# Performance work log

Hardware: AMD Instinct MI355X
Metric: run time of the kernel (lower is better)

The kernel has to match this reference:

```python
import jax, jax.numpy as jnp
import numpy as np

# --- Mamba2Simple hyperparams (derived from init_kwargs) ---
D_MODEL = 2048
D_STATE = 128
HEADDIM = 64
EXPAND = 2
D_CONV = 4
NGROUPS = 1
CHUNK = 256
EPS = 1e-5
D_INNER = EXPAND * D_MODEL            # 4096
NHEADS = D_INNER // HEADDIM           # 64
CONV_DIM = D_INNER + 2 * NGROUPS * D_STATE          # 4352
D_IN_PROJ = 2 * D_INNER + 2 * NGROUPS * D_STATE + NHEADS  # 8512


def setup_inputs() -> dict:
    key = jax.random.key(0)
    ks = jax.random.split(key, 9)
    B, L = 2, 2048
    x = jax.random.normal(ks[0], (B, L, D_MODEL), jnp.float32)
    w_in = jax.random.normal(ks[1], (D_MODEL, D_IN_PROJ), jnp.float32) * (D_MODEL ** -0.5)
    conv_w = jax.random.normal(ks[2], (CONV_DIM, D_CONV), jnp.float32) * 0.2
    conv_b = jnp.zeros((CONV_DIM,), jnp.float32)
    dt_bias = jax.random.uniform(ks[3], (NHEADS,), jnp.float32, -4.0, -1.0)
    # A in [1, 16] per official init -> A_log = log(A)
    A_log = jnp.log(jax.random.uniform(ks[4], (NHEADS,), jnp.float32, 1.0, 16.0))
    D = jnp.ones((NHEADS,), jnp.float32)
    norm_w = jnp.ones((D_INNER,), jnp.float32)
    w_out = jax.random.normal(ks[5], (D_INNER, D_MODEL), jnp.float32) * (D_INNER ** -0.5)
    return {"x": x, "w_in": w_in, "conv_w": conv_w, "conv_b": conv_b,
            "dt_bias": dt_bias, "A_log": A_log, "D": D, "norm_w": norm_w, "w_out": w_out}


def _segsum(a):
    # a: (..., T) -> (..., T, T) with out[i, j] = sum_{k=j+1..i} a[k] for j<=i else -inf
    T = a.shape[-1]
    cs = jnp.cumsum(a, axis=-1)
    d = cs[..., :, None] - cs[..., None, :]
    mask = jnp.tril(jnp.ones((T, T), dtype=bool))
    return jnp.where(mask, d, -jnp.inf)


def _ssd(X, A, Bm, Cm):
    # X: (b, l, h, p) already multiplied by dt; A: (b, l, h) = dt*A_cont
    # Bm, Cm: (b, l, n)  (ngroups=1, broadcast over heads)
    b, l, h, p = X.shape
    n = Bm.shape[-1]
    c = l // CHUNK
    X = X.reshape(b, c, CHUNK, h, p)
    A = A.reshape(b, c, CHUNK, h).transpose(0, 3, 1, 2)      # (b, h, c, q)
    Bm = Bm.reshape(b, c, CHUNK, n)
    Cm = Cm.reshape(b, c, CHUNK, n)
    A_cs = jnp.cumsum(A, axis=-1)                             # (b, h, c, q)
    Lmat = jnp.exp(_segsum(A))                                # (b, h, c, q, q)
    # intra-chunk (diagonal block) output
    Y_diag = jnp.einsum("bcln,bcsn,bhcls,bcshp->bclhp", Cm, Bm, Lmat, X)
    # per-chunk final states
    decay_states = jnp.exp(A_cs[..., -1:] - A_cs)             # (b, h, c, q)
    states = jnp.einsum("bcln,bhcl,bclhp->bchpn", Bm, decay_states, X)
    # inter-chunk recurrence
    A_last = jnp.pad(A_cs[..., -1], ((0, 0), (0, 0), (1, 0)))  # (b, h, c+1)
    decay_chunk = jnp.exp(_segsum(A_last))                     # (b, h, c+1, c+1)
    states = jnp.concatenate([jnp.zeros_like(states[:, :1]), states], axis=1)
    states = jnp.einsum("bhzc,bchpn->bzhpn", decay_chunk, states)[:, :-1]
    # state -> output contribution
    Y_off = jnp.einsum("bchpn,bcln,bhcl->bclhp", states, Cm, jnp.exp(A_cs))
    return (Y_diag + Y_off).reshape(b, l, h, p)


def _mamba2(x, w_in, conv_w, conv_b, dt_bias, A_log, D, norm_w, w_out):
    B, L, _ = x.shape
    zxbcdt = jnp.einsum("bld,de->ble", x, w_in)               # (B, L, 8512)
    z = zxbcdt[..., :D_INNER]
    xBC = zxbcdt[..., D_INNER:D_INNER + CONV_DIM]
    dt = zxbcdt[..., D_INNER + CONV_DIM:]                      # (B, L, H)
    dt = jax.nn.softplus(dt + dt_bias)
    # causal depthwise conv1d + silu
    xp = jnp.pad(xBC, ((0, 0), (D_CONV - 1, 0), (0, 0)))
    acc = conv_b
    xBC = sum(conv_w[:, k] * xp[:, k:k + L, :] for k in range(D_CONV)) + conv_b
    xBC = jax.nn.silu(xBC)
    xh = xBC[..., :D_INNER].reshape(B, L, NHEADS, HEADDIM)
    Bm = xBC[..., D_INNER:D_INNER + NGROUPS * D_STATE]         # (B, L, N) since ngroups=1
    Cm = xBC[..., D_INNER + NGROUPS * D_STATE:]                # (B, L, N)
    A = -jnp.exp(A_log)                                        # (H,)
    y = _ssd(xh * dt[..., None], dt * A, Bm, Cm)               # (B, L, H, P)
    y = y + xh * D[None, None, :, None]                        # skip term
    y = y.reshape(B, L, D_INNER)
    # gated RMSNorm (norm_before_gate=False): normalize(y * silu(z)) * weight
    y = y * jax.nn.silu(z)
    y = y * jax.lax.rsqrt(jnp.mean(y * y, axis=-1, keepdims=True) + EPS) * norm_w
    return jnp.einsum("ble,ed->bld", y, w_out)


def reference(x, w_in, conv_w, conv_b, dt_bias, A_log, D, norm_w, w_out):
    return x + _mamba2(x, w_in, conv_w, conv_b, dt_bias, A_log, D, norm_w, w_out)
```

## Files before the change

kernel.cpp:

```cpp
#include <hip/hip_runtime.h>
#include <math.h>

#define DEV __device__ __forceinline__

typedef __attribute__((ext_vector_type(4))) float f32x4;
typedef __attribute__((ext_vector_type(4))) unsigned short u16x4;
typedef __attribute__((ext_vector_type(8))) unsigned short u16x8;
typedef __attribute__((ext_vector_type(8))) __bf16 bfv8;

DEV unsigned short f2bf(float f) {
  unsigned u = __builtin_bit_cast(unsigned, f);
  u = (u + 0x7FFFu + ((u >> 16) & 1u)) >> 16;
  return (unsigned short)u;
}
DEV float bf2f(unsigned short h) {
  unsigned u = ((unsigned)h) << 16;
  return __builtin_bit_cast(float, u);
}

DEV f32x4 mfma16(u16x8 a, u16x8 b, f32x4 c) {
  return __builtin_amdgcn_mfma_f32_16x16x32_bf16(
      __builtin_bit_cast(bfv8, a), __builtin_bit_cast(bfv8, b), c, 0, 0, 0);
}

DEV void gload_lds16(const unsigned short* g, unsigned short* s) {
  __builtin_amdgcn_global_load_lds(
      (const __attribute__((address_space(1))) void*)g,
      (__attribute__((address_space(3))) void*)s, 16, 0, 0);
}

template <int N>
DEV void vmcnt_wait() {
  if constexpr (N == 0) asm volatile("s_waitcnt vmcnt(0)" ::: "memory");
  else if constexpr (N == 2) asm volatile("s_waitcnt vmcnt(2)" ::: "memory");
  else if constexpr (N == 4) asm volatile("s_waitcnt vmcnt(4)" ::: "memory");
}

__global__ __launch_bounds__(512, 2) void gemm8_in(
    const unsigned short* __restrict__ A, const unsigned short* __restrict__ Bt,
    unsigned short* __restrict__ o_z, unsigned short* __restrict__ o_xbc,
    float* __restrict__ o_dt) {
  constexpr int K = 2048, NT = K / 64;
  __shared__ __align__(16) unsigned short As[2][256 * 64];
  __shared__ __align__(16) unsigned short Bs[2][256 * 64];
  const int tid = threadIdx.x;
  const int lane = tid & 63, w = tid >> 6;
  const int l16 = lane & 15, lq = lane >> 4;
  const int wr = w >> 1, wc = w & 1;
  const int nwg = gridDim.x * gridDim.y;
  int lin = blockIdx.y * gridDim.x + blockIdx.x;
  lin = (lin & 7) * (nwg >> 3) + (lin >> 3);
  const int m0 = (lin / gridDim.x) * 256, n0 = (lin % gridDim.x) * 256;
  const int srow = lane >> 3;
  const int schk = (lane & 7) ^ srow;
  const unsigned short* Ag = A + (size_t)(m0 + srow) * K + schk * 8;
  const unsigned short* Bg = Bt + (size_t)(n0 + srow) * K + schk * 8;
  const int px0 = lq ^ (l16 & 7);
  const int px1 = (4 + lq) ^ (l16 & 7);

  f32x4 acc[4][8] = {};

  auto stageA = [&](int p, int slot, int kt) {
    gload_lds16(Ag + (size_t)(slot * 64 + w * 8) * K + kt * 64,
                &As[p][(slot * 64 + w * 8) * 64]);
  };
  auto stageB = [&](int p, int slot, int kt) {
    gload_lds16(Bg + (size_t)(slot * 64 + w * 8) * K + kt * 64,
                &Bs[p][(slot * 64 + w * 8) * 64]);
  };
  auto rdA = [&](int p, int mf, int k2) -> u16x8 {
    const int row = wr * 64 + mf * 16 + l16;
    return *(const u16x8*)(&As[p][row * 64 + (k2 ? px1 : px0) * 8]);
  };
  auto rdB = [&](int p, int nf, int k2) -> u16x8 {
    const int row = wc * 128 + nf * 16 + l16;
    return *(const u16x8*)(&Bs[p][row * 64 + (k2 ? px1 : px0) * 8]);
  };

  stageA(0, 0, 0); stageA(0, 1, 0); stageA(0, 2, 0); stageA(0, 3, 0);
  stageB(0, 0, 0); stageB(0, 2, 0); stageB(0, 1, 0); stageB(0, 3, 0);
  vmcnt_wait<2>();
  __builtin_amdgcn_s_barrier();

  u16x8 a0[4], a1[4], b0[2], b1[2];
  for (int k = 0; k < NT; ++k) {
    const int p = k & 1, pn = p ^ 1;
    const bool st = (k + 1 < NT);
#pragma unroll
    for (int mf = 0; mf < 4; ++mf) { a0[mf] = rdA(p, mf, 0); a1[mf] = rdA(p, mf, 1); }
    b0[0] = rdB(p, 0, 0); b1[0] = rdB(p, 0, 1);
    b0[1] = rdB(p, 1, 0); b1[1] = rdB(p, 1, 1);
    if (st) { stageA(pn, 0, k + 1); stageA(pn, 1, k + 1); }
    __builtin_amdgcn_s_barrier();
    __builtin_amdgcn_s_setprio(1);
#pragma unroll
    for (int nf = 0; nf < 2; ++nf)
#pragma unroll
      for (int mf = 0; mf < 4; ++mf) {
        acc[mf][nf] = mfma16(a0[mf], b0[nf], acc[mf][nf]);
        acc[mf][nf] = mfma16(a1[mf], b1[nf], acc[mf][nf]);
      }
    __builtin_amdgcn_s_setprio(0);
    __builtin_amdgcn_s_barrier();
    b0[0] = rdB(p, 2, 0); b1[0] = rdB(p, 2, 1);
    b0[1] = rdB(p, 3, 0); b1[1] = rdB(p, 3, 1);
    if (st) { stageA(pn, 2, k + 1); stageA(pn, 3, k + 1); vmcnt_wait<4>(); }
    else vmcnt_wait<0>();
    __builtin_amdgcn_s_barrier();
    __builtin_amdgcn_s_setprio(1);
#pragma unroll
    for (int nf = 0; nf < 2; ++nf)
#pragma unroll
      for (int mf = 0; mf < 4; ++mf) {
        acc[mf][2 + nf] = mfma16(a0[mf], b0[nf], acc[mf][2 + nf]);
        acc[mf][2 + nf] = mfma16(a1[mf], b1[nf], acc[mf][2 + nf]);
      }
    __builtin_amdgcn_s_setprio(0);
    __builtin_amdgcn_s_barrier();
    b0[0] = rdB(p, 4, 0); b1[0] = rdB(p, 4, 1);
    b0[1] = rdB(p, 5, 0); b1[1] = rdB(p, 5, 1);
    if (st) { stageB(pn, 0, k + 1); stageB(pn, 2, k + 1); }
    __builtin_amdgcn_s_barrier();
    __builtin_amdgcn_s_setprio(1);
#pragma unroll
    for (int nf = 0; nf < 2; ++nf)
#pragma unroll
      for (int mf = 0; mf < 4; ++mf) {
        acc[mf][4 + nf] = mfma16(a0[mf], b0[nf], acc[mf][4 + nf]);
        acc[mf][4 + nf] = mfma16(a1[mf], b1[nf], acc[mf][4 + nf]);
      }
    __builtin_amdgcn_s_setprio(0);
    __builtin_amdgcn_s_barrier();
    b0[0] = rdB(p, 6, 0); b1[0] = rdB(p, 6, 1);
    b0[1] = rdB(p, 7, 0); b1[1] = rdB(p, 7, 1);
    if (st) { stageB(pn, 1, k + 1); stageB(pn, 3, k + 1); vmcnt_wait<2>(); }
    else vmcnt_wait<0>();
    __builtin_amdgcn_s_barrier();
    __builtin_amdgcn_s_setprio(1);
#pragma unroll
    for (int nf = 0; nf < 2; ++nf)
#pragma unroll
      for (int mf = 0; mf < 4; ++mf) {
        acc[mf][6 + nf] = mfma16(a0[mf], b0[nf], acc[mf][6 + nf]);
        acc[mf][6 + nf] = mfma16(a1[mf], b1[nf], acc[mf][6 + nf]);
      }
    __builtin_amdgcn_s_setprio(0);
    __builtin_amdgcn_s_barrier();
  }

#pragma unroll
  for (int mf = 0; mf < 4; ++mf) {
#pragma unroll
    for (int nf = 0; nf < 8; ++nf) {
      const int col = n0 + wc * 128 + nf * 16 + l16;
#pragma unroll
      for (int r = 0; r < 4; ++r) {
        const int row = m0 + wr * 64 + mf * 16 + lq * 4 + r;
        float v = acc[mf][nf][r];
        if (col < 4096) o_z[(size_t)row * 4096 + col] = f2bf(v);
        else if (col < 8448) o_xbc[(size_t)row * 4352 + (col - 4096)] = f2bf(v);
        else if (col < 8512) o_dt[(size_t)row * 64 + (col - 8448)] = v;
      }
    }
  }
}

__global__ __launch_bounds__(256, 3) void gemm_p(
    const unsigned short* __restrict__ A, const unsigned short* __restrict__ Bt,
    int K, float* __restrict__ o_c, const float* __restrict__ resid) {
  __shared__ __align__(16) unsigned short As[3][128 * 32];
  __shared__ __align__(16) unsigned short Bs[3][128 * 32];
  const int tid = threadIdx.x;
  const int lane = tid & 63, w = tid >> 6;
  const int l16 = lane & 15, lq = lane >> 4;
  const int wr = w >> 1, wc = w & 1;
  const int nwg = gridDim.x * gridDim.y;
  int lin = blockIdx.y * gridDim.x + blockIdx.x;
  lin = (lin & 7) * (nwg >> 3) + (lin >> 3);
  const int m0 = (lin / gridDim.x) * 128, n0 = (lin % gridDim.x) * 128;
  const int lrow = lane >> 2;
  const int gq = (lane & 3) ^ ((lrow >> 1) & 3);
  const int cq = lq ^ ((l16 >> 1) & 3);

  const unsigned short* Ag = A + (size_t)(m0 + lrow) * K + gq * 8;
  const unsigned short* Bg = Bt + (size_t)(n0 + lrow) * K + gq * 8;

  f32x4 acc[4][4] = {};

  auto stage = [&](int bi, int kt) {
#pragma unroll
    for (int i = 0; i < 2; ++i) {
      const int rb = (w + i * 4) * 16;
      gload_lds16(Ag + (size_t)rb * K + kt * 32, &As[bi][rb * 32]);
    }
#pragma unroll
    for (int i = 0; i < 2; ++i) {
      const int rb = (w + i * 4) * 16;
      gload_lds16(Bg + (size_t)rb * K + kt * 32, &Bs[bi][rb * 32]);
    }
  };

  const int nt = K / 32;
  stage(0, 0);
  stage(1, 1);

  for (int k = 0; k < nt; ++k) {
    const int cb = k % 3;
    if (k < nt - 1) vmcnt_wait<4>();
    else vmcnt_wait<0>();
    __builtin_amdgcn_s_barrier();
    if (k + 2 < nt) stage((k + 2) % 3, k + 2);

    u16x8 af[4], bf[4];
#pragma unroll
    for (int mf = 0; mf < 4; ++mf)
      af[mf] = *(const u16x8*)(&As[cb][(wr * 64 + mf * 16 + l16) * 32 + cq * 8]);
#pragma unroll
    for (int nf = 0; nf < 4; ++nf)
      bf[nf] = *(const u16x8*)(&Bs[cb][(wc * 64 + nf * 16 + l16) * 32 + cq * 8]);

    __builtin_amdgcn_s_setprio(1);
#pragma unroll
    for (int mf = 0; mf < 4; ++mf)
#pragma unroll
      for (int nf = 0; nf < 4; ++nf)
        acc[mf][nf] = mfma16(af[mf], bf[nf], acc[mf][nf]);
    __builtin_amdgcn_s_setprio(0);
  }

#pragma unroll
  for (int mf = 0; mf < 4; ++mf) {
#pragma unroll
    for (int nf = 0; nf < 4; ++nf) {
      const int col = n0 + wc * 64 + nf * 16 + l16;
#pragma unroll
      for (int r = 0; r < 4; ++r) {
        const int row = m0 + wr * 64 + mf * 16 + lq * 4 + r;
        size_t idx = (size_t)row * 2048 + col;
        o_c[idx] = acc[mf][nf][r] + resid[idx];
      }
    }
  }
}

__global__ __launch_bounds__(256) void prep_kernel(
    const float* __restrict__ x, unsigned short* __restrict__ xbf,
    const float* __restrict__ w_in, unsigned short* __restrict__ w_inT) {
  __shared__ __align__(16) unsigned short T[64][72];
  const int b = blockIdx.x;
  const int tid = threadIdx.x;
  if (b < 4096) {
    const size_t i = ((size_t)b * 256 + tid) * 8;
    f32x4 a = *(const f32x4*)(x + i);
    f32x4 c = *(const f32x4*)(x + i + 4);
    u16x8 o;
#pragma unroll
    for (int j = 0; j < 4; ++j) { o[j] = f2bf(a[j]); o[j + 4] = f2bf(c[j]); }
    *(u16x8*)(xbf + i) = o;
  } else {
    const int idx = b - 4096;
    const int c0 = (idx % 136) * 64, r0 = (idx / 136) * 64;
#pragma unroll
    for (int it = 0; it < 4; ++it) {
      int r = it * 16 + (tid >> 4);
      int c = (tid & 15) * 4;
      f32x4 v = {0.f, 0.f, 0.f, 0.f};
      if (c0 + c < 8512) v = *(const f32x4*)(w_in + (size_t)(r0 + r) * 8512 + c0 + c);
#pragma unroll
      for (int j = 0; j < 4; ++j) T[c + j][r] = f2bf(v[j]);
    }
    __syncthreads();
    const int nr = tid >> 2, kc = (tid & 3) * 16;
    u16x8 a = *(const u16x8*)(&T[nr][kc]);
    u16x8 c = *(const u16x8*)(&T[nr][kc + 8]);
    unsigned short* o = w_inT + (size_t)(c0 + nr) * 2048 + r0 + kc;
    *(u16x8*)o = a;
    *(u16x8*)(o + 8) = c;
  }
}

__global__ __launch_bounds__(256) void transpose_conv(
    const float* __restrict__ in, unsigned short* __restrict__ out, int R,
    int C) {
  __shared__ __align__(16) unsigned short T[64][72];
  const int c0 = blockIdx.x * 64, r0 = blockIdx.y * 64;
  const int tid = threadIdx.x;
#pragma unroll
  for (int it = 0; it < 4; ++it) {
    int r = it * 16 + (tid >> 4);
    int c = (tid & 15) * 4;
    f32x4 v = {0.f, 0.f, 0.f, 0.f};
    if (c0 + c < C) v = *(const f32x4*)(in + (size_t)(r0 + r) * C + c0 + c);
#pragma unroll
    for (int j = 0; j < 4; ++j) T[c + j][r] = f2bf(v[j]);
  }
  __syncthreads();
  const int nr = tid >> 2, kc = (tid & 3) * 16;
  u16x8 a = *(const u16x8*)(&T[nr][kc]);
  u16x8 b = *(const u16x8*)(&T[nr][kc + 8]);
  unsigned short* o = out + (size_t)(c0 + nr) * R + r0 + kc;
  *(u16x8*)o = a;
  *(u16x8*)(o + 8) = b;
}

__global__ __launch_bounds__(256) void convdt_kernel(
    const unsigned short* __restrict__ raw, const float* __restrict__ cw,
    const float* __restrict__ cb, unsigned short* __restrict__ xbc,
    float* __restrict__ dtb, const float* __restrict__ dt_bias,
    const float* __restrict__ A_log, float* __restrict__ Acs) {
  __shared__ float wsum[4];
  const int b = blockIdx.x;
  const int tid = threadIdx.x;
  if (b < 5120) {
    const int ch4 = (b % 5) * 256 + tid;
    if (ch4 >= 1088) return;
    const int ch = ch4 * 4;
    const int r0 = (b / 5) * 4;
    const int l0 = r0 & 2047;
    f32x4 w0 = *(const f32x4*)(cw + ch * 4);
    f32x4 w1 = *(const f32x4*)(cw + ch * 4 + 4);
    f32x4 w2 = *(const f32x4*)(cw + ch * 4 + 8);
    f32x4 w3 = *(const f32x4*)(cw + ch * 4 + 12);
    f32x4 bias = *(const f32x4*)(cb + ch);
    f32x4 v[7];
#pragma unroll
    for (int i = 0; i < 7; ++i) {
      if (l0 - 3 + i >= 0) {
        u16x4 h = *(const u16x4*)(raw + (size_t)(r0 - 3 + i) * 4352 + ch);
        v[i] = (f32x4){bf2f(h[0]), bf2f(h[1]), bf2f(h[2]), bf2f(h[3])};
      } else {
        v[i] = (f32x4){0.f, 0.f, 0.f, 0.f};
      }
    }
#pragma unroll
    for (int j = 0; j < 4; ++j) {
      f32x4 acc = bias;
#pragma unroll
      for (int k = 0; k < 4; ++k) {
        acc[0] += w0[k] * v[j + k][0];
        acc[1] += w1[k] * v[j + k][1];
        acc[2] += w2[k] * v[j + k][2];
        acc[3] += w3[k] * v[j + k][3];
      }
      u16x4 o;
#pragma unroll
      for (int q = 0; q < 4; ++q) {
        float s = acc[q] / (1.0f + __expf(-acc[q]));
        o[q] = f2bf(s);
      }
      *(u16x4*)(xbc + (size_t)(r0 + j) * 4352 + ch) = o;
    }
  } else {
    const int blk = b - 5120;
    const int c = blk & 7, h = (blk >> 3) & 63, bb = blk >> 9;
    const int lane = tid & 63, w = tid >> 6;
    const int row = bb * 2048 + c * 256 + tid;
    float xv = dtb[(size_t)row * 64 + h] + dt_bias[h];
    float dt = (xv > 20.0f) ? xv : log1pf(__expf(xv));
    dtb[(size_t)row * 64 + h] = dt;
    float s = dt * (-__expf(A_log[h]));
#pragma unroll
    for (int off = 1; off < 64; off <<= 1) {
      float v = __shfl_up(s, off, 64);
      if (lane >= off) s += v;
    }
    if (lane == 63) wsum[w] = s;
    __syncthreads();
    float base = 0.0f;
#pragma unroll
    for (int i = 0; i < 4; ++i)
      if (i < w) base += wsum[i];
    Acs[((size_t)((bb * 64 + h) * 8 + c)) * 256 + tid] = s + base;
  }
}

__global__ __launch_bounds__(256) void g_kernel(
    const unsigned short* __restrict__ xbc, float* __restrict__ G) {
  const int bc = blockIdx.y;
  const int i0 = (blockIdx.x >> 2) * 64, j0 = (blockIdx.x & 3) * 64;
  const int tid = threadIdx.x;
  const int lane = tid & 63, w = tid >> 6;
  const int l16 = lane & 15, lq = lane >> 4;
  const unsigned short* base = xbc + (size_t)bc * 256 * 4352;
  f32x4 acc[4] = {};
#pragma unroll
  for (int ks = 0; ks < 4; ++ks) {
    int nb = ks * 32 + lq * 8;
    u16x8 af = *(const u16x8*)(base + (size_t)(i0 + w * 16 + l16) * 4352 + 4224 + nb);
#pragma unroll
    for (int jf = 0; jf < 4; ++jf) {
      u16x8 bb = *(const u16x8*)(base + (size_t)(j0 + jf * 16 + l16) * 4352 + 4096 + nb);
      acc[jf] = mfma16(af, bb, acc[jf]);
    }
  }
  float* Gt = G + (size_t)bc * 65536;
#pragma unroll
  for (int jf = 0; jf < 4; ++jf)
#pragma unroll
    for (int r = 0; r < 4; ++r)
      Gt[(i0 + w * 16 + lq * 4 + r) * 256 + j0 + jf * 16 + l16] = acc[jf][r];
}

__global__ __launch_bounds__(512) void ssd_states(
    const unsigned short* __restrict__ xbc, const float* __restrict__ dtb,
    const float* __restrict__ Acs, unsigned short* __restrict__ statesb) {
  __shared__ __align__(16) unsigned short Xt[64 * 264];
  __shared__ __align__(16) unsigned short BmT[128 * 72];
  __shared__ float As_s[256];
  const int h = blockIdx.x, c = blockIdx.y, b = blockIdx.z;
  const int tid = threadIdx.x;
  const int lane = tid & 63, w = tid >> 6;
  const int l16 = lane & 15, lq = lane >> 4;
  const int row0 = b * 2048 + c * 256;

  if (tid < 256) As_s[tid] = Acs[((size_t)((b * 64 + h) * 8 + c)) * 256 + tid];
#pragma unroll
  for (int it = 0; it < 2; ++it) {
    int pb = tid & 15;
    int tb = it * 32 + (tid >> 4);
    float rr[4][4];
#pragma unroll
    for (int i = 0; i < 4; ++i) {
      int row = row0 + tb * 4 + i;
      u16x4 v = *(const u16x4*)(xbc + (size_t)row * 4352 + h * 64 + pb * 4);
      float dtv = dtb[(size_t)row * 64 + h];
#pragma unroll
      for (int j = 0; j < 4; ++j) rr[i][j] = bf2f(v[j]) * dtv;
    }
#pragma unroll
    for (int j = 0; j < 4; ++j) {
      u16x4 hh = {f2bf(rr[0][j]), f2bf(rr[1][j]), f2bf(rr[2][j]), f2bf(rr[3][j])};
      *(u16x4*)(&Xt[(pb * 4 + j) * 264 + tb * 4]) = hh;
    }
  }
  __syncthreads();

  f32x4 accS[4] = {};
  const float Alast = As_s[255];
  for (int part = 0; part < 4; ++part) {
    if (part) __syncthreads();
    {
      int nb = tid & 31;
      int tb = tid >> 5;
      float rr[4][4];
#pragma unroll
      for (int i = 0; i < 4; ++i) {
        int t = part * 64 + tb * 4 + i;
        int row = row0 + t;
        float dec = __expf(Alast - As_s[t]);
        u16x4 v = *(const u16x4*)(xbc + (size_t)row * 4352 + 4096 + nb * 4);
#pragma unroll
        for (int j = 0; j < 4; ++j) rr[i][j] = bf2f(v[j]) * dec;
      }
#pragma unroll
      for (int j = 0; j < 4; ++j) {
        u16x4 hh = {f2bf(rr[0][j]), f2bf(rr[1][j]), f2bf(rr[2][j]), f2bf(rr[3][j])};
        *(u16x4*)(&BmT[(nb * 4 + j) * 72 + tb * 4]) = hh;
      }
    }
    __syncthreads();
#pragma unroll
    for (int ks = 0; ks < 2; ++ks) {
      int toff = ks * 32 + lq * 8;
      u16x8 af = *(const u16x8*)(&BmT[(w * 16 + l16) * 72 + toff]);
#pragma unroll
      for (int pf = 0; pf < 4; ++pf) {
        u16x8 bfr = *(const u16x8*)(&Xt[(pf * 16 + l16) * 264 + part * 64 + toff]);
        accS[pf] = mfma16(af, bfr, accS[pf]);
      }
    }
  }
  unsigned short* Sp = statesb + (size_t)((b * 8 + c) * 64 + h) * 8192;
#pragma unroll
  for (int pf = 0; pf < 4; ++pf) {
    u16x4 hh = {f2bf(accS[pf][0]), f2bf(accS[pf][1]), f2bf(accS[pf][2]),
                f2bf(accS[pf][3])};
    *(u16x4*)(&Sp[(pf * 16 + l16) * 128 + w * 16 + lq * 4]) = hh;
  }
}

__global__ __launch_bounds__(256) void scan_states(
    const unsigned short* __restrict__ statesb, const float* __restrict__ Acs,
    unsigned short* __restrict__ prefix) {
  const int h = blockIdx.x, b = blockIdx.y;
  const int tid = threadIdx.x;
  const int p = tid >> 2, nq = (tid & 3) * 32;
  float S[32];
#pragma unroll
  for (int i = 0; i < 32; ++i) S[i] = 0.0f;
  for (int cc = 0; cc < 8; ++cc) {
    size_t base = (size_t)((b * 8 + cc) * 64 + h) * 8192 + p * 128 + nq;
#pragma unroll
    for (int j = 0; j < 4; ++j) {
      u16x8 hh;
#pragma unroll
      for (int k = 0; k < 8; ++k) hh[k] = f2bf(S[j * 8 + k]);
      *(u16x8*)(prefix + base + j * 8) = hh;
    }
    float eAl = __expf(Acs[((size_t)((b * 64 + h) * 8 + cc)) * 256 + 255]);
#pragma unroll
    for (int j = 0; j < 4; ++j) {
      u16x8 v = *(const u16x8*)(statesb + base + j * 8);
#pragma unroll
      for (int k = 0; k < 8; ++k) S[j * 8 + k] = eAl * S[j * 8 + k] + bf2f(v[k]);
    }
  }
}

__global__ __launch_bounds__(512) void ssd_main(
    const unsigned short* __restrict__ xbc, const float* __restrict__ dtb,
    const float* __restrict__ Acs, const float* __restrict__ G,
    const unsigned short* __restrict__ prefix, const float* __restrict__ Dv,
    unsigned short* __restrict__ y) {
  __shared__ __align__(16) unsigned short Xt[64 * 264];
  __shared__ float As_s[256];
  const int h = blockIdx.x, c = blockIdx.y, b = blockIdx.z;
  const int tid = threadIdx.x;
  const int lane = tid & 63, w = tid >> 6;
  const int l16 = lane & 15, lq = lane >> 4;
  const int row0 = b * 2048 + c * 256;

  if (tid < 256) As_s[tid] = Acs[((size_t)((b * 64 + h) * 8 + c)) * 256 + tid];
#pragma unroll
  for (int it = 0; it < 2; ++it) {
    int pb = tid & 15;
    int tb = it * 32 + (tid >> 4);
    float rr[4][4];
#pragma unroll
    for (int i = 0; i < 4; ++i) {
      int row = row0 + tb * 4 + i;
      u16x4 v = *(const u16x4*)(xbc + (size_t)row * 4352 + h * 64 + pb * 4);
      float dtv = dtb[(size_t)row * 64 + h];
#pragma unroll
      for (int j = 0; j < 4; ++j) rr[i][j] = bf2f(v[j]) * dtv;
    }
#pragma unroll
    for (int j = 0; j < 4; ++j) {
      u16x4 hh = {f2bf(rr[0][j]), f2bf(rr[1][j]), f2bf(rr[2][j]), f2bf(rr[3][j])};
      *(u16x4*)(&Xt[(pb * 4 + j) * 264 + tb * 4]) = hh;
    }
  }
  __syncthreads();

  f32x4 acc[2][4] = {};
  const float* Gt = G + (size_t)(b * 8 + c) * 65536;
  for (int ks = 0; ks < 8; ++ks) {
    const int tb = ks * 32 + lq * 8;
    u16x8 bfr[4];
#pragma unroll
    for (int pf = 0; pf < 4; ++pf)
      bfr[pf] = *(const u16x8*)(&Xt[(pf * 16 + l16) * 264 + tb]);
#pragma unroll
    for (int mf = 0; mf < 2; ++mf) {
      const int i = w * 32 + mf * 16 + l16;
      const float ai = As_s[i];
      const float* gp = Gt + i * 256 + tb;
      f32x4 g0 = *(const f32x4*)gp;
      f32x4 g1 = *(const f32x4*)(gp + 4);
      u16x8 af;
#pragma unroll
      for (int jj = 0; jj < 8; ++jj) {
        int j = tb + jj;
        float g = (jj < 4) ? g0[jj] : g1[jj - 4];
        float v = (i >= j) ? g * __expf(ai - As_s[j]) : 0.0f;
        af[jj] = f2bf(v);
      }
#pragma unroll
      for (int pf = 0; pf < 4; ++pf)
        acc[mf][pf] = mfma16(af, bfr[pf], acc[mf][pf]);
    }
  }
  const unsigned short* Pf = prefix + (size_t)((b * 8 + c) * 64 + h) * 8192;
  for (int ks = 0; ks < 4; ++ks) {
    const int nb = ks * 32 + lq * 8;
    u16x8 bfr[4];
#pragma unroll
    for (int pf = 0; pf < 4; ++pf)
      bfr[pf] = *(const u16x8*)(Pf + (size_t)(pf * 16 + l16) * 128 + nb);
#pragma unroll
    for (int mf = 0; mf < 2; ++mf) {
      const int i = w * 32 + mf * 16 + l16;
      const float eAi = __expf(As_s[i]);
      u16x8 cv = *(const u16x8*)(xbc + (size_t)(row0 + i) * 4352 + 4224 + nb);
      u16x8 af;
#pragma unroll
      for (int jj = 0; jj < 8; ++jj) af[jj] = f2bf(bf2f(cv[jj]) * eAi);
#pragma unroll
      for (int pf = 0; pf < 4; ++pf)
        acc[mf][pf] = mfma16(af, bfr[pf], acc[mf][pf]);
    }
  }
  const float Dh = Dv[h];
#pragma unroll
  for (int mf = 0; mf < 2; ++mf) {
#pragma unroll
    for (int r = 0; r < 4; ++r) {
      int t = w * 32 + mf * 16 + lq * 4 + r;
      size_t row = (size_t)(row0 + t);
#pragma unroll
      for (int pf = 0; pf < 4; ++pf) {
        int p = pf * 16 + l16;
        float xh = bf2f(xbc[row * 4352 + h * 64 + p]);
        y[row * 4096 + h * 64 + p] = f2bf(acc[mf][pf][r] + Dh * xh);
      }
    }
  }
}

__global__ __launch_bounds__(256) void norm_kernel(
    unsigned short* __restrict__ y, const unsigned short* __restrict__ zbf,
    const float* __restrict__ nw) {
  const int row = blockIdx.x, tid = threadIdx.x;
  unsigned short* yr = y + (size_t)row * 4096;
  const unsigned short* zr = zbf + (size_t)row * 4096;
  float vals[16];
  float ss = 0.0f;
#pragma unroll
  for (int i = 0; i < 2; ++i) {
    int cb = i * 2048 + tid * 8;
    u16x8 yv = *(const u16x8*)(yr + cb);
    u16x8 zv = *(const u16x8*)(zr + cb);
#pragma unroll
    for (int j = 0; j < 8; ++j) {
      float z = bf2f(zv[j]);
      float g = bf2f(yv[j]) * (z / (1.0f + __expf(-z)));
      vals[i * 8 + j] = g;
      ss += g * g;
    }
  }
#pragma unroll
  for (int off = 32; off > 0; off >>= 1) ss += __shfl_xor(ss, off, 64);
  __shared__ float red[4];
  if ((tid & 63) == 0) red[tid >> 6] = ss;
  __syncthreads();
  float tot = red[0] + red[1] + red[2] + red[3];
  float rr = rsqrtf(tot * (1.0f / 4096.0f) + 1e-5f);
#pragma unroll
  for (int i = 0; i < 2; ++i) {
    int cb = i * 2048 + tid * 8;
    f32x4 w0 = *(const f32x4*)(nw + cb);
    f32x4 w1 = *(const f32x4*)(nw + cb + 4);
    u16x8 o;
#pragma unroll
    for (int j = 0; j < 8; ++j) {
      float wv = (j < 4) ? w0[j] : w1[j - 4];
      o[j] = f2bf(vals[i * 8 + j] * rr * wv);
    }
    *(u16x8*)(yr + cb) = o;
  }
}

extern "C" void kernel_launch(void* const* d_in, const int* in_sizes, int n_in,
                              void* d_out, int out_size, void* d_ws,
                              size_t ws_size, hipStream_t stream) {
  const float* x = (const float*)d_in[0];
  const float* w_in = (const float*)d_in[1];
  const float* conv_w = (const float*)d_in[2];
  const float* conv_b = (const float*)d_in[3];
  const float* dt_bias = (const float*)d_in[4];
  const float* A_log = (const float*)d_in[5];
  const float* Dvec = (const float*)d_in[6];
  const float* norm_w = (const float*)d_in[7];
  const float* w_out = (const float*)d_in[8];
  float* out = (float*)d_out;

  char* w = (char*)d_ws;
  unsigned short* zbf = (unsigned short*)(w + 0);
  unsigned short* xbc = (unsigned short*)(w + 33554432);
  unsigned short* xbcraw = (unsigned short*)(w + 69206016);
  float* dtb = (float*)(w + 104857600);
  float* Acs = (float*)(w + 105906176);
  float* G = (float*)(w + 106954752);
  unsigned short* statesb = (unsigned short*)(w + 111149056);
  unsigned short* y = (unsigned short*)(w + 127926272);
  unsigned short* xbf = (unsigned short*)(w + 111149056);
  unsigned short* w_inT = (unsigned short*)(w + 33554432);
  unsigned short* w_outT = (unsigned short*)(w + 33554432);
  unsigned short* prefix = xbcraw;

  prep_kernel<<<dim3(8448), 256, 0, stream>>>(x, xbf, w_in, w_inT);
  gemm8_in<<<dim3(34, 16), 512, 0, stream>>>(xbf, w_inT, zbf, xbcraw, dtb);
  convdt_kernel<<<dim3(6144), 256, 0, stream>>>(xbcraw, conv_w, conv_b, xbc,
                                                dtb, dt_bias, A_log, Acs);
  g_kernel<<<dim3(16, 16), 256, 0, stream>>>(xbc, G);
  ssd_states<<<dim3(64, 8, 2), 512, 0, stream>>>(xbc, dtb, Acs, statesb);
  scan_states<<<dim3(64, 2), 256, 0, stream>>>(statesb, Acs, prefix);
  ssd_main<<<dim3(64, 8, 2), 512, 0, stream>>>(xbc, dtb, Acs, G, prefix, Dvec, y);
  transpose_conv<<<dim3(32, 64), 256, 0, stream>>>(w_out, w_outT, 4096, 2048);
  norm_kernel<<<dim3(4096), 256, 0, stream>>>(y, zbf, norm_w);
  gemm_p<<<dim3(16, 32), 256, 0, stream>>>(y, w_outT, 4096, out, x);
}
```

Measured before the change: 460.7 us.

## Store G in bf16, split state scan across N halves, fuse norm with w_out transpose

The intra-chunk C·B^T matrix G is now written and read as bf16 instead of fp32, halving its memory traffic in g_kernel and ssd_main. The state scan is split into two blocks per head along the state dimension, doubling parallelism with fewer registers per thread. The w_out transpose is merged into the RMSNorm launch as extra blocks, removing one kernel launch and letting both run concurrently. Rounding G to bf16 adds a small precision loss before the decay multiply.

Result: faster. 436.4 us (-5.3%).

```diff
diff --git a/kernel.cpp b/kernel.cpp
--- a/kernel.cpp
+++ b/kernel.cpp
@@ -279,30 +279,6 @@
   }
 }
 
-__global__ __launch_bounds__(256) void transpose_conv(
-    const float* __restrict__ in, unsigned short* __restrict__ out, int R,
-    int C) {
-  __shared__ __align__(16) unsigned short T[64][72];
-  const int c0 = blockIdx.x * 64, r0 = blockIdx.y * 64;
-  const int tid = threadIdx.x;
-#pragma unroll
-  for (int it = 0; it < 4; ++it) {
-    int r = it * 16 + (tid >> 4);
-    int c = (tid & 15) * 4;
-    f32x4 v = {0.f, 0.f, 0.f, 0.f};
-    if (c0 + c < C) v = *(const f32x4*)(in + (size_t)(r0 + r) * C + c0 + c);
-#pragma unroll
-    for (int j = 0; j < 4; ++j) T[c + j][r] = f2bf(v[j]);
-  }
-  __syncthreads();
-  const int nr = tid >> 2, kc = (tid & 3) * 16;
-  u16x8 a = *(const u16x8*)(&T[nr][kc]);
-  u16x8 b = *(const u16x8*)(&T[nr][kc + 8]);
-  unsigned short* o = out + (size_t)(c0 + nr) * R + r0 + kc;
-  *(u16x8*)o = a;
-  *(u16x8*)(o + 8) = b;
-}
-
 __global__ __launch_bounds__(256) void convdt_kernel(
     const unsigned short* __restrict__ raw, const float* __restrict__ cw,
     const float* __restrict__ cb, unsigned short* __restrict__ xbc,
@@ -375,7 +351,7 @@
 }
 
 __global__ __launch_bounds__(256) void g_kernel(
-    const unsigned short* __restrict__ xbc, float* __restrict__ G) {
+    const unsigned short* __restrict__ xbc, unsigned short* __restrict__ G) {
   const int bc = blockIdx.y;
   const int i0 = (blockIdx.x >> 2) * 64, j0 = (blockIdx.x & 3) * 64;
   const int tid = threadIdx.x;
@@ -393,12 +369,13 @@
       acc[jf] = mfma16(af, bb, acc[jf]);
     }
   }
-  float* Gt = G + (size_t)bc * 65536;
+  unsigned short* Gt = G + (size_t)bc * 65536;
 #pragma unroll
   for (int jf = 0; jf < 4; ++jf)
 #pragma unroll
     for (int r = 0; r < 4; ++r)
-      Gt[(i0 + w * 16 + lq * 4 + r) * 256 + j0 + jf * 16 + l16] = acc[jf][r];
+      Gt[(i0 + w * 16 + lq * 4 + r) * 256 + j0 + jf * 16 + l16] =
+          f2bf(acc[jf][r]);
 }
 
 __global__ __launch_bounds__(512) void ssd_states(
@@ -482,16 +459,16 @@
 __global__ __launch_bounds__(256) void scan_states(
     const unsigned short* __restrict__ statesb, const float* __restrict__ Acs,
     unsigned short* __restrict__ prefix) {
-  const int h = blockIdx.x, b = blockIdx.y;
-  const int tid = threadIdx.x;
-  const int p = tid >> 2, nq = (tid & 3) * 32;
-  float S[32];
-#pragma unroll
-  for (int i = 0; i < 32; ++i) S[i] = 0.0f;
+  const int h = blockIdx.x, b = blockIdx.y, nh = blockIdx.z;
+  const int tid = threadIdx.x;
+  const int p = tid >> 2, nq = nh * 64 + (tid & 3) * 16;
+  float S[16];
+#pragma unroll
+  for (int i = 0; i < 16; ++i) S[i] = 0.0f;
   for (int cc = 0; cc < 8; ++cc) {
     size_t base = (size_t)((b * 8 + cc) * 64 + h) * 8192 + p * 128 + nq;
 #pragma unroll
-    for (int j = 0; j < 4; ++j) {
+    for (int j = 0; j < 2; ++j) {
       u16x8 hh;
 #pragma unroll
       for (int k = 0; k < 8; ++k) hh[k] = f2bf(S[j * 8 + k]);
@@ -499,7 +476,7 @@
     }
     float eAl = __expf(Acs[((size_t)((b * 64 + h) * 8 + cc)) * 256 + 255]);
 #pragma unroll
-    for (int j = 0; j < 4; ++j) {
+    for (int j = 0; j < 2; ++j) {
       u16x8 v = *(const u16x8*)(statesb + base + j * 8);
 #pragma unroll
       for (int k = 0; k < 8; ++k) S[j * 8 + k] = eAl * S[j * 8 + k] + bf2f(v[k]);
@@ -509,7 +486,7 @@
 
 __global__ __launch_bounds__(512) void ssd_main(
     const unsigned short* __restrict__ xbc, const float* __restrict__ dtb,
-    const float* __restrict__ Acs, const float* __restrict__ G,
+    const float* __restrict__ Acs, const unsigned short* __restrict__ G,
     const unsigned short* __restrict__ prefix, const float* __restrict__ Dv,
     unsigned short* __restrict__ y) {
   __shared__ __align__(16) unsigned short Xt[64 * 264];
@@ -543,7 +520,7 @@
   __syncthreads();
 
   f32x4 acc[2][4] = {};
-  const float* Gt = G + (size_t)(b * 8 + c) * 65536;
+  const unsigned short* Gt = G + (size_t)(b * 8 + c) * 65536;
   for (int ks = 0; ks < 8; ++ks) {
     const int tb = ks * 32 + lq * 8;
     u16x8 bfr[4];
@@ -554,15 +531,12 @@
     for (int mf = 0; mf < 2; ++mf) {
       const int i = w * 32 + mf * 16 + l16;
       const float ai = As_s[i];
-      const float* gp = Gt + i * 256 + tb;
-      f32x4 g0 = *(const f32x4*)gp;
-      f32x4 g1 = *(const f32x4*)(gp + 4);
+      u16x8 gv = *(const u16x8*)(Gt + (size_t)i * 256 + tb);
       u16x8 af;
 #pragma unroll
       for (int jj = 0; jj < 8; ++jj) {
         int j = tb + jj;
-        float g = (jj < 4) ? g0[jj] : g1[jj - 4];
-        float v = (i >= j) ? g * __expf(ai - As_s[j]) : 0.0f;
+        float v = (i >= j) ? bf2f(gv[jj]) * __expf(ai - As_s[j]) : 0.0f;
         af[jj] = f2bf(v);
       }
 #pragma unroll
@@ -607,46 +581,69 @@
   }
 }
 
-__global__ __launch_bounds__(256) void norm_kernel(
+__global__ __launch_bounds__(256) void norm_trans(
     unsigned short* __restrict__ y, const unsigned short* __restrict__ zbf,
-    const float* __restrict__ nw) {
-  const int row = blockIdx.x, tid = threadIdx.x;
-  unsigned short* yr = y + (size_t)row * 4096;
-  const unsigned short* zr = zbf + (size_t)row * 4096;
-  float vals[16];
-  float ss = 0.0f;
-#pragma unroll
-  for (int i = 0; i < 2; ++i) {
-    int cb = i * 2048 + tid * 8;
-    u16x8 yv = *(const u16x8*)(yr + cb);
-    u16x8 zv = *(const u16x8*)(zr + cb);
-#pragma unroll
-    for (int j = 0; j < 8; ++j) {
-      float z = bf2f(zv[j]);
-      float g = bf2f(yv[j]) * (z / (1.0f + __expf(-z)));
-      vals[i * 8 + j] = g;
-      ss += g * g;
-    }
-  }
-#pragma unroll
-  for (int off = 32; off > 0; off >>= 1) ss += __shfl_xor(ss, off, 64);
+    const float* __restrict__ nw, const float* __restrict__ w_out,
+    unsigned short* __restrict__ w_outT) {
+  __shared__ __align__(16) unsigned short T[64][72];
   __shared__ float red[4];
-  if ((tid & 63) == 0) red[tid >> 6] = ss;
-  __syncthreads();
-  float tot = red[0] + red[1] + red[2] + red[3];
-  float rr = rsqrtf(tot * (1.0f / 4096.0f) + 1e-5f);
-#pragma unroll
-  for (int i = 0; i < 2; ++i) {
-    int cb = i * 2048 + tid * 8;
-    f32x4 w0 = *(const f32x4*)(nw + cb);
-    f32x4 w1 = *(const f32x4*)(nw + cb + 4);
-    u16x8 o;
-#pragma unroll
-    for (int j = 0; j < 8; ++j) {
-      float wv = (j < 4) ? w0[j] : w1[j - 4];
-      o[j] = f2bf(vals[i * 8 + j] * rr * wv);
-    }
-    *(u16x8*)(yr + cb) = o;
+  const int b = blockIdx.x;
+  const int tid = threadIdx.x;
+  if (b < 4096) {
+    unsigned short* yr = y + (size_t)b * 4096;
+    const unsigned short* zr = zbf + (size_t)b * 4096;
+    float vals[16];
+    float ss = 0.0f;
+#pragma unroll
+    for (int i = 0; i < 2; ++i) {
+      int cb = i * 2048 + tid * 8;
+      u16x8 yv = *(const u16x8*)(yr + cb);
+      u16x8 zv = *(const u16x8*)(zr + cb);
+#pragma unroll
+      for (int j = 0; j < 8; ++j) {
+        float z = bf2f(zv[j]);
+        float g = bf2f(yv[j]) * (z / (1.0f + __expf(-z)));
+        vals[i * 8 + j] = g;
+        ss += g * g;
+      }
+    }
+#pragma unroll
+    for (int off = 32; off > 0; off >>= 1) ss += __shfl_xor(ss, off, 64);
+    if ((tid & 63) == 0) red[tid >> 6] = ss;
+    __syncthreads();
+    float tot = red[0] + red[1] + red[2] + red[3];
+    float rr = rsqrtf(tot * (1.0f / 4096.0f) + 1e-5f);
+#pragma unroll
+    for (int i = 0; i < 2; ++i) {
+      int cb = i * 2048 + tid * 8;
+      f32x4 w0 = *(const f32x4*)(nw + cb);
+      f32x4 w1 = *(const f32x4*)(nw + cb + 4);
+      u16x8 o;
+#pragma unroll
+      for (int j = 0; j < 8; ++j) {
+        float wv = (j < 4) ? w0[j] : w1[j - 4];
+        o[j] = f2bf(vals[i * 8 + j] * rr * wv);
+      }
+      *(u16x8*)(yr + cb) = o;
+    }
+  } else {
+    const int idx = b - 4096;
+    const int c0 = (idx & 31) * 64, r0 = (idx >> 5) * 64;
+#pragma unroll
+    for (int it = 0; it < 4; ++it) {
+      int r = it * 16 + (tid >> 4);
+      int c = (tid & 15) * 4;
+      f32x4 v = *(const f32x4*)(w_out + (size_t)(r0 + r) * 2048 + c0 + c);
+#pragma unroll
+      for (int j = 0; j < 4; ++j) T[c + j][r] = f2bf(v[j]);
+    }
+    __syncthreads();
+    const int nr = tid >> 2, kc = (tid & 3) * 16;
+    u16x8 a = *(const u16x8*)(&T[nr][kc]);
+    u16x8 c = *(const u16x8*)(&T[nr][kc + 8]);
+    unsigned short* o = w_outT + (size_t)(c0 + nr) * 4096 + r0 + kc;
+    *(u16x8*)o = a;
+    *(u16x8*)(o + 8) = c;
   }
 }
 
@@ -670,7 +667,7 @@
   unsigned short* xbcraw = (unsigned short*)(w + 69206016);
   float* dtb = (float*)(w + 104857600);
   float* Acs = (float*)(w + 105906176);
-  float* G = (float*)(w + 106954752);
+  unsigned short* G = (unsigned short*)(w + 106954752);
   unsigned short* statesb = (unsigned short*)(w + 111149056);
   unsigned short* y = (unsigned short*)(w + 127926272);
   unsigned short* xbf = (unsigned short*)(w + 111149056);
@@ -684,9 +681,8 @@
                                                 dtb, dt_bias, A_log, Acs);
   g_kernel<<<dim3(16, 16), 256, 0, stream>>>(xbc, G);
   ssd_states<<<dim3(64, 8, 2), 512, 0, stream>>>(xbc, dtb, Acs, statesb);
-  scan_states<<<dim3(64, 2), 256, 0, stream>>>(statesb, Acs, prefix);
+  scan_states<<<dim3(64, 2, 2), 256, 0, stream>>>(statesb, Acs, prefix);
   ssd_main<<<dim3(64, 8, 2), 512, 0, stream>>>(xbc, dtb, Acs, G, prefix, Dvec, y);
-  transpose_conv<<<dim3(32, 64), 256, 0, stream>>>(w_out, w_outT, 4096, 2048);
-  norm_kernel<<<dim3(4096), 256, 0, stream>>>(y, zbf, norm_w);
+  norm_trans<<<dim3(6144), 256, 0, stream>>>(y, zbf, norm_w, w_out, w_outT);
   gemm_p<<<dim3(16, 32), 256, 0, stream>>>(y, w_outT, 4096, out, x);
 }
```
